# Kernel optimization log

Hardware: AMD Instinct MI355X
Metric: run time of the kernel (lower is better)

The kernel has to match this reference:

```python
import jax, jax.numpy as jnp
import numpy as np

T_LEN, BATCH, HID = 1024, 8, 1024
TEMP = 0.1
EPS = 1e-12  # torch F.normalize eps


def setup_inputs() -> dict:
    key = jax.random.key(0)
    k1, k2, k3, k4 = jax.random.split(key, 4)
    h1 = jax.random.normal(k1, (T_LEN, BATCH, HID), jnp.float32)
    h2 = jax.random.normal(k2, (T_LEN, BATCH, HID), jnp.float32)
    # learned params of nn.Sequential(Linear, ReLU, Linear, ReLU)
    W1 = jax.random.normal(k3, (HID, HID), jnp.float32) * 0.02
    b1 = jnp.zeros((HID,), jnp.float32)
    W2 = jax.random.normal(k4, (HID, HID), jnp.float32) * 0.02
    b2 = jnp.zeros((HID,), jnp.float32)
    return {"h1": h1, "h2": h2, "W1": W1, "b1": b1, "W2": W2, "b2": b2}


def _mlp(x, W1, b1, W2, b2):
    x = jax.nn.relu(x @ W1 + b1)
    return jax.nn.relu(x @ W2 + b2)


def _info_nce(emb_i, emb_j, temperature=TEMP):
    # emb_i, emb_j: [n, h] with n = 2*(t-1)
    n = emb_i.shape[0]
    z_i = emb_i / jnp.maximum(jnp.linalg.norm(emb_i, axis=1, keepdims=True), EPS)
    z_j = emb_j / jnp.maximum(jnp.linalg.norm(emb_j, axis=1, keepdims=True), EPS)
    reps = jnp.concatenate([z_i, z_j], axis=0)          # [2n, h]
    sim = reps @ reps.T                                  # cosine sim (rows are unit)
    logits = sim / temperature
    exp_l = jnp.exp(logits)
    # denominator excludes self-similarity (scatter of 0 at position i)
    denom = exp_l.sum(axis=1) - jnp.diagonal(exp_l)      # [2n]
    log_denom = jnp.log(denom)
    idx = jnp.arange(n)
    l_ab = -logits[idx, idx + n] + log_denom[:n]         # l(k, k+N)
    l_ba = -logits[idx + n, idx] + log_denom[n:]         # l(k+N, k)
    return (l_ab.sum() + l_ba.sum()) / (2.0 * n)


def reference(h1, h2, W1, b1, W2, b2):
    h1 = jnp.transpose(h1, (1, 0, 2))  # [b, t, h]
    h2 = jnp.transpose(h2, (1, 0, 2))
    h1 = _mlp(h1, W1, b1, W2, b2)
    h2 = _mlp(h2, W1, b1, W2, b2)
    h_t_1 = jnp.concatenate([h1[:, 1:, :], h2[:, 1:, :]], axis=1)    # [b, 2(t-1), h]
    h_t_2 = jnp.concatenate([h1[:, :-1, :], h2[:, :-1, :]], axis=1)
    # original loop overwrites cl_loss each iteration -> only last batch row counts
    cl_loss = _info_nce(h_t_1[-1], h_t_2[-1])
    return (h1, h2, cl_loss)
```

## Files before the change

### kernel.cpp

```cpp
#include <hip/hip_runtime.h>
#include <cstdint>
#include <cstddef>

using u16 = unsigned short;
using u8  = unsigned char;
typedef short short8 __attribute__((ext_vector_type(8)));
typedef __bf16 bf16x8 __attribute__((ext_vector_type(8)));
typedef float f32x4 __attribute__((ext_vector_type(4)));
typedef u16 u16x4 __attribute__((ext_vector_type(4)));
typedef int i32x4 __attribute__((ext_vector_type(4)));
typedef int i32x8 __attribute__((ext_vector_type(8)));

__device__ __forceinline__ u16 f2bf(float f) {
  union { float f; uint32_t u; } v; v.f = f;
  uint32_t r = v.u + 0x7FFF + ((v.u >> 16) & 1);
  return (u16)(r >> 16);
}
__device__ __forceinline__ float bf2f(u16 b) {
  union { uint32_t u; float f; } v; v.u = ((uint32_t)b) << 16;
  return v.f;
}
__device__ __forceinline__ u8 f2fp8(float f) {
  return (u8)(__builtin_amdgcn_cvt_pk_fp8_f32(f, f, 0, 0) & 0xFF);
}

__device__ __forceinline__ void gload16(const void* g, void* l) {
  __builtin_amdgcn_global_load_lds(
      (const __attribute__((address_space(1))) void*)g,
      (__attribute__((address_space(3))) void*)l, 16, 0, 0);
}

#define MFMAQ8(M0, N0, AF, BF)                                             \
  {                                                                        \
    _Pragma("unroll") for (int m_ = 0; m_ < 4; ++m_) {                     \
      _Pragma("unroll") for (int n_ = 0; n_ < 2; ++n_) {                   \
        acc[(M0) + m_][(N0) + n_] =                                        \
            __builtin_amdgcn_mfma_scale_f32_16x16x128_f8f6f4(              \
                AF[m_], BF[n_], acc[(M0) + m_][(N0) + n_],                 \
                0, 0, 0, 127, 0, 127);                                     \
      }                                                                    \
    }                                                                      \
  }

template <int EPI>
__global__ __launch_bounds__(512, 2) void gemm_fp8(
    const u8* __restrict__ A, const u8* __restrict__ Bt,
    const float* __restrict__ bias,
    u8* __restrict__ C8, float* __restrict__ Cf)
{
  constexpr int Kb = 1024, N = 1024, NT = 8;
  __shared__ alignas(16) u8 lds[131072];

  const int t = (int)threadIdx.x;
  const int lane = t & 63, wid = t >> 6;
  const int wr = wid >> 2, wc = wid & 3;
  const int li = lane & 15, hk = lane >> 4;

  const int orig = (int)blockIdx.x;
  const int cpx = (int)gridDim.x >> 3;
  const int swz = (orig & 7) * cpx + (orig >> 3);
  const int bm = swz >> 2, bn = swz & 3;
  const int arow0 = bm * 256, brow0 = bn * 256;

  const int Rl = lane >> 3;
  const int sc16 = ((lane & 7) ^ Rl) << 4;
  const int wid2 = wid * 2;

  const int c0b = (((hk << 1) + 0) ^ (li & 7)) << 4;
  const int c1b = (((hk << 1) + 1) ^ (li & 7)) << 4;

  f32x4 acc[8][4];
#pragma unroll
  for (int m = 0; m < 8; ++m)
#pragma unroll
    for (int n = 0; n < 4; ++n)
#pragma unroll
      for (int j = 0; j < 4; ++j) acc[m][n][j] = 0.0f;

  auto STAGE = [&](const u8* G, int growbase, int tau, int ldsoff) {
#pragma unroll
    for (int l = 0; l < 2; ++l) {
      const u8* g = G + (size_t)(growbase + (wid2 + l) * 8 + Rl) * Kb +
                    tau * 128 + sc16;
      gload16(g, lds + ldsoff + (wid2 + l) * 1024);
    }
  };
  auto RD = [&](const u8* base, int row) -> i32x8 {
    const u8* p = base + row * 128;
    i32x4 lo = *reinterpret_cast<const i32x4*>(p + c0b);
    i32x4 hi = *reinterpret_cast<const i32x4*>(p + c1b);
    i32x8 r;
    r[0] = lo[0]; r[1] = lo[1]; r[2] = lo[2]; r[3] = lo[3];
    r[4] = hi[0]; r[5] = hi[1]; r[6] = hi[2]; r[7] = hi[3];
    return r;
  };

  i32x8 aa[4], bb01[2], bb23[2];

  STAGE(Bt, brow0 + 0,   0, 65536 + 0);
  STAGE(Bt, brow0 + 128, 0, 65536 + 16384);
  STAGE(A,  arow0 + 0,   0, 0);
  STAGE(A,  arow0 + 128, 0, 16384);
  STAGE(Bt, brow0 + 0,   1, 65536 + 32768);
  STAGE(Bt, brow0 + 128, 1, 65536 + 32768 + 16384);
  STAGE(A,  arow0 + 0,   1, 32768);
  STAGE(A,  arow0 + 128, 1, 32768 + 16384);
  asm volatile("s_waitcnt vmcnt(8)" ::: "memory");
  __builtin_amdgcn_s_barrier();

  {
    const u8* Ab0 = lds + wr * 16384;
    const u8* Bb0 = lds + 65536 + wc * 8192;
#pragma unroll
    for (int m = 0; m < 4; ++m) aa[m] = RD(Ab0, m * 16 + li);
#pragma unroll
    for (int n = 0; n < 2; ++n) bb01[n] = RD(Bb0, n * 16 + li);
  }

  for (int tau = 0; tau < NT; ++tau) {
    const int cur = tau & 1, nxt = cur ^ 1;
    const u8* Ab  = lds + cur * 32768 + wr * 16384;
    const u8* Bb  = lds + 65536 + cur * 32768 + wc * 8192;
    const u8* Abn = lds + nxt * 32768 + wr * 16384;
    const u8* Bbn = lds + 65536 + nxt * 32768 + wc * 8192;

#pragma unroll
    for (int n = 0; n < 2; ++n) bb23[n] = RD(Bb, 32 + n * 16 + li);
    asm volatile("s_waitcnt lgkmcnt(4)" ::: "memory");
    __builtin_amdgcn_sched_barrier(0);
    __builtin_amdgcn_s_setprio(1);
    MFMAQ8(0, 0, aa, bb01);
    __builtin_amdgcn_s_setprio(0);

    asm volatile("s_waitcnt lgkmcnt(0)" ::: "memory");
    __builtin_amdgcn_sched_barrier(0);
    __builtin_amdgcn_s_setprio(1);
    MFMAQ8(0, 2, aa, bb23);
    __builtin_amdgcn_s_setprio(0);
    __builtin_amdgcn_sched_barrier(0);
#pragma unroll
    for (int m = 0; m < 4; ++m) aa[m] = RD(Ab, (m + 4) * 16 + li);
    __builtin_amdgcn_s_barrier();

    if (tau + 2 < NT) {
      STAGE(Bt, brow0 + 0,   tau + 2, 65536 + cur * 32768);
      STAGE(Bt, brow0 + 128, tau + 2, 65536 + cur * 32768 + 16384);
    }
    asm volatile("s_waitcnt lgkmcnt(0)" ::: "memory");
    __builtin_amdgcn_sched_barrier(0);
    __builtin_amdgcn_s_setprio(1);
    MFMAQ8(4, 2, aa, bb23);
    __builtin_amdgcn_s_setprio(0);
    __builtin_amdgcn_s_barrier();

    if (tau + 2 < NT) {
      STAGE(A, arow0 + 0,   tau + 2, cur * 32768);
      STAGE(A, arow0 + 128, tau + 2, cur * 32768 + 16384);
      asm volatile("s_waitcnt vmcnt(8)" ::: "memory");
    } else if (tau + 1 < NT) {
      asm volatile("s_waitcnt vmcnt(0)" ::: "memory");
    }
    __builtin_amdgcn_s_barrier();
    __builtin_amdgcn_s_setprio(1);
    MFMAQ8(4, 0, aa, bb01);
    __builtin_amdgcn_s_setprio(0);
    __builtin_amdgcn_sched_barrier(0);
    if (tau + 1 < NT) {
#pragma unroll
      for (int m = 0; m < 4; ++m) aa[m] = RD(Abn, m * 16 + li);
#pragma unroll
      for (int n = 0; n < 2; ++n) bb01[n] = RD(Bbn, n * 16 + li);
    }
  }

#pragma unroll
  for (int m = 0; m < 8; ++m) {
#pragma unroll
    for (int n = 0; n < 4; ++n) {
      const int gcol = brow0 + wc * 64 + n * 16 + li;
      const float bv = bias[gcol];
#pragma unroll
      for (int j = 0; j < 4; ++j) {
        const int grow = arow0 + wr * 128 + m * 16 + hk * 4 + j;
        float v = fmaxf(acc[m][n][j] * 0.001953125f + bv, 0.0f);
        if (EPI == 0) {
          C8[(size_t)grow * N + gcol] = f2fp8(v * 8.0f);
        } else {
          int tensor = grow >> 13, rr = grow & 8191;
          int tt = rr >> 3, b_ = rr & 7;
          Cf[(size_t)tensor * 8388608 + (size_t)b_ * 1048576 +
             (size_t)tt * 1024 + gcol] = v;
        }
      }
    }
  }
}

__global__ __launch_bounds__(256) void sim_kernel(const u16* __restrict__ Z,
                                                  float* __restrict__ S,
                                                  float* __restrict__ dots)
{
  __shared__ alignas(16) u16 As[128 * 128];
  __shared__ alignas(16) u16 Bs[128 * 128];
  const int t = (int)threadIdx.x;
  const int lane = t & 63, wv = t >> 6;
  const int wr = wv >> 1, wc = wv & 1;
  const int li = lane & 15, hk = lane >> 4;
  const int sr = t >> 4;
  const int scc = t & 15;
  const int bm = (int)blockIdx.x >> 4, bn = (int)blockIdx.x & 15;
  const int arow0 = bm * 128, brow0 = bn * 128;

  f32x4 acc[4][4];
#pragma unroll
  for (int m = 0; m < 4; ++m)
#pragma unroll
    for (int n = 0; n < 4; ++n)
#pragma unroll
      for (int j = 0; j < 4; ++j) acc[m][n][j] = 0.0f;

  for (int kt = 0; kt < 1024; kt += 128) {
#pragma unroll
    for (int l = 0; l < 8; ++l) {
      int row = l * 16 + sr;
      int coff = (scc ^ (row & 7)) << 3;
      const u16* ga = Z + (size_t)(arow0 + row) * 1024 + kt + coff;
      const u16* gb = Z + (size_t)(brow0 + row) * 1024 + kt + coff;
      gload16(ga, As + l * 2048 + wv * 512);
      gload16(gb, Bs + l * 2048 + wv * 512);
    }
    __syncthreads();
#pragma unroll
    for (int kk = 0; kk < 4; ++kk) {
      short8 av[4], bv[4];
#pragma unroll
      for (int m = 0; m < 4; ++m) {
        int ra = wr * 64 + m * 16 + li;
        int ca = ((kk << 2) + hk) ^ (ra & 7);
        av[m] = *reinterpret_cast<const short8*>(As + ra * 128 + ca * 8);
      }
#pragma unroll
      for (int n = 0; n < 4; ++n) {
        int rb = wc * 64 + n * 16 + li;
        int cb = ((kk << 2) + hk) ^ (rb & 7);
        bv[n] = *reinterpret_cast<const short8*>(Bs + rb * 128 + cb * 8);
      }
#pragma unroll
      for (int m = 0; m < 4; ++m)
#pragma unroll
        for (int n = 0; n < 4; ++n)
          acc[m][n] = __builtin_amdgcn_mfma_f32_16x16x32_bf16(
              __builtin_bit_cast(bf16x8, av[m]),
              __builtin_bit_cast(bf16x8, bv[n]),
              acc[m][n], 0, 0, 0);
    }
    __syncthreads();
  }

  float dsum = 0.0f;
#pragma unroll
  for (int m = 0; m < 4; ++m) {
#pragma unroll
    for (int j = 0; j < 4; ++j) {
      int grow = arow0 + wr * 64 + m * 16 + hk * 4 + j;
      float s = 0.0f;
#pragma unroll
      for (int n = 0; n < 4; ++n) {
        int gcol = brow0 + wc * 64 + n * 16 + li;
        float g = acc[m][n][j];
        float logit = (grow == gcol) ? 10.0f : g * 10.0f;
        float w = (gcol == 0 || gcol == 1023 || gcol == 1024 || gcol == 2047)
                      ? 1.0f : 2.0f;
        s += w * expf(logit);
        if (gcol == grow + 1 && (grow & 1023) != 1023) dsum += g;
      }
      s += __shfl_xor(s, 1); s += __shfl_xor(s, 2);
      s += __shfl_xor(s, 4); s += __shfl_xor(s, 8);
      if (li == 0) atomicAdd(&S[grow], s);
    }
  }
#pragma unroll
  for (int d = 1; d < 64; d <<= 1) dsum += __shfl_xor(dsum, d);
  if (lane == 0) atomicAdd(dots, dsum);
}

__global__ void prep_kernel(const float* __restrict__ h1,
                            const float* __restrict__ h2,
                            const float* __restrict__ W1,
                            const float* __restrict__ W2,
                            u8* __restrict__ X8,
                            u8* __restrict__ W1t,
                            u8* __restrict__ W2t,
                            float* __restrict__ S)
{
  __shared__ float tile[32][33];
  int bid = (int)blockIdx.x;
  if (bid < 16384) {
    size_t i4 = ((size_t)bid * 256 + threadIdx.x) * 4;
    const float* src = (i4 < 8388608) ? (h1 + i4) : (h2 + (i4 - 8388608));
    float4 v = *reinterpret_cast<const float4*>(src);
    int lo = __builtin_amdgcn_cvt_pk_fp8_f32(v.x * 8.0f, v.y * 8.0f, 0, 0);
    int all4 = __builtin_amdgcn_cvt_pk_fp8_f32(v.z * 8.0f, v.w * 8.0f, lo, 1);
    *reinterpret_cast<uint32_t*>(X8 + i4) = (uint32_t)all4;
    return;
  }
  bid -= 16384;
  const float* W;
  u8* Wt;
  if (bid < 1024) {
    W = W1; Wt = W1t;
  } else if (bid < 2048) {
    W = W2; Wt = W2t; bid -= 1024;
  } else {
    for (int i = (int)threadIdx.x; i < 2064; i += 256) S[i] = 0.0f;
    return;
  }
  const int bx = bid & 31, by = bid >> 5;
  const int tx = (int)threadIdx.x & 31, ty = (int)threadIdx.x >> 5;
#pragma unroll
  for (int i = 0; i < 4; ++i)
    tile[ty + i * 8][tx] = W[(size_t)(by * 32 + ty + i * 8) * 1024 + bx * 32 + tx];
  __syncthreads();
#pragma unroll
  for (int i = 0; i < 4; ++i)
    Wt[(size_t)(bx * 32 + ty + i * 8) * 1024 + by * 32 + tx] =
        f2fp8(tile[tx][ty + i * 8] * 64.0f);
}

__global__ void row_normalize(const float* __restrict__ out, u16* __restrict__ Z)
{
  const int row = (int)blockIdx.x;
  const int t = (int)threadIdx.x;
  const float* src = out + ((row < 1024)
      ? ((size_t)7 * 1048576 + (size_t)row * 1024)
      : ((size_t)8388608 + (size_t)7 * 1048576 + (size_t)(row - 1024) * 1024));
  float4 v = reinterpret_cast<const float4*>(src)[t];
  float ss = v.x * v.x + v.y * v.y + v.z * v.z + v.w * v.w;
#pragma unroll
  for (int d = 1; d < 64; d <<= 1) ss += __shfl_xor(ss, d);
  __shared__ float red[4];
  if ((t & 63) == 0) red[t >> 6] = ss;
  __syncthreads();
  float tot = red[0] + red[1] + red[2] + red[3];
  float inv = 1.0f / fmaxf(sqrtf(tot), 1e-12f);
  u16x4 o;
  o[0] = f2bf(v.x * inv); o[1] = f2bf(v.y * inv);
  o[2] = f2bf(v.z * inv); o[3] = f2bf(v.w * inv);
  reinterpret_cast<u16x4*>(Z + (size_t)row * 1024)[t] = o;
}

__global__ void finalize_kernel(const float* __restrict__ S,
                                const float* __restrict__ dots,
                                float* __restrict__ out_loss)
{
  const int t = (int)threadIdx.x;
  float acc = 0.0f;
  for (int i = t; i < 2048; i += 256) {
    int tl = i & 1023;
    float w = (tl == 0 || tl == 1023) ? 1.0f : 2.0f;
    acc += w * logf(S[i] - 22026.465794806718f);
  }
  __shared__ float red[256];
  red[t] = acc;
  __syncthreads();
  for (int s2 = 128; s2 > 0; s2 >>= 1) {
    if (t < s2) red[t] += red[t + s2];
    __syncthreads();
  }
  if (t == 0) out_loss[0] = (red[0] - 20.0f * dots[0]) / 4092.0f;
}

extern "C" void kernel_launch(void* const* d_in, const int* in_sizes, int n_in,
                              void* d_out, int out_size, void* d_ws, size_t ws_size,
                              hipStream_t stream)
{
  const float* h1 = (const float*)d_in[0];
  const float* h2 = (const float*)d_in[1];
  const float* W1 = (const float*)d_in[2];
  const float* b1 = (const float*)d_in[3];
  const float* W2 = (const float*)d_in[4];
  const float* b2 = (const float*)d_in[5];
  float* out = (float*)d_out;

  char* ws = (char*)d_ws;
  u8*    X8   = (u8*)ws;
  u8*    Y18  = (u8*)(ws + 16777216);
  u8*    W1t  = (u8*)(ws + 33554432);
  u8*    W2t  = (u8*)(ws + 34603008);
  u16*   Zb   = (u16*)(ws + 35651584);
  float* S    = (float*)(ws + 39845888);
  float* dots = S + 2048;

  prep_kernel<<<18433, 256, 0, stream>>>(h1, h2, W1, W2, X8, W1t, W2t, S);

  gemm_fp8<0><<<256, 512, 0, stream>>>(X8, W1t, b1, Y18, nullptr);
  gemm_fp8<1><<<256, 512, 0, stream>>>(Y18, W2t, b2, nullptr, out);

  row_normalize<<<2048, 256, 0, stream>>>(out, Zb);
  sim_kernel<<<256, 256, 0, stream>>>(Zb, S, dots);
  finalize_kernel<<<1, 256, 0, stream>>>(S, dots, out + 16777216);
}
```

Measured before the change: 104.3 us.

## Run the InfoNCE similarity GEMM in FP8 using the shared pipelined GEMM core

Row-normalized embeddings are now quantized to FP8 with a 16x scale instead of bf16, and the similarity matrix is computed by a new sim_fp8 kernel. This kernel reuses the pipelined FP8 MFMA core, factored out of gemm_fp8, with 256x256 tiles over 64 blocks of 512 threads. The goal is to halve the bytes the similarity kernel loads and to use the higher-throughput FP8 MFMA with the better-tuned pipeline. The risk is lower precision in the cosine similarities that feed the exp/log loss, and only 64 blocks on a GPU with many more compute units.

Result: slower. 193.6 us (+85.6%).

```diff
diff --git a/kernel.cpp b/kernel.cpp
--- a/kernel.cpp
+++ b/kernel.cpp
@@ -15,10 +15,6 @@
   union { float f; uint32_t u; } v; v.f = f;
   uint32_t r = v.u + 0x7FFF + ((v.u >> 16) & 1);
   return (u16)(r >> 16);
-}
-__device__ __forceinline__ float bf2f(u16 b) {
-  union { uint32_t u; float f; } v; v.u = ((uint32_t)b) << 16;
-  return v.f;
 }
 __device__ __forceinline__ u8 f2fp8(float f) {
   return (u8)(__builtin_amdgcn_cvt_pk_fp8_f32(f, f, 0, 0) & 0xFF);
@@ -42,40 +38,18 @@
     }                                                                      \
   }
 
-template <int EPI>
-__global__ __launch_bounds__(512, 2) void gemm_fp8(
+__device__ __forceinline__ void fp8_core(
     const u8* __restrict__ A, const u8* __restrict__ Bt,
-    const float* __restrict__ bias,
-    u8* __restrict__ C8, float* __restrict__ Cf)
-{
-  constexpr int Kb = 1024, N = 1024, NT = 8;
-  __shared__ alignas(16) u8 lds[131072];
-
-  const int t = (int)threadIdx.x;
-  const int lane = t & 63, wid = t >> 6;
-  const int wr = wid >> 2, wc = wid & 3;
-  const int li = lane & 15, hk = lane >> 4;
-
-  const int orig = (int)blockIdx.x;
-  const int cpx = (int)gridDim.x >> 3;
-  const int swz = (orig & 7) * cpx + (orig >> 3);
-  const int bm = swz >> 2, bn = swz & 3;
-  const int arow0 = bm * 256, brow0 = bn * 256;
-
+    int arow0, int brow0, u8* lds, f32x4 (&acc)[8][4],
+    int lane, int wid, int wr, int wc, int li)
+{
+  constexpr int Kb = 1024, NT = 8;
   const int Rl = lane >> 3;
   const int sc16 = ((lane & 7) ^ Rl) << 4;
   const int wid2 = wid * 2;
-
+  const int hk = lane >> 4;
   const int c0b = (((hk << 1) + 0) ^ (li & 7)) << 4;
   const int c1b = (((hk << 1) + 1) ^ (li & 7)) << 4;
-
-  f32x4 acc[8][4];
-#pragma unroll
-  for (int m = 0; m < 8; ++m)
-#pragma unroll
-    for (int n = 0; n < 4; ++n)
-#pragma unroll
-      for (int j = 0; j < 4; ++j) acc[m][n][j] = 0.0f;
 
   auto STAGE = [&](const u8* G, int growbase, int tau, int ldsoff) {
 #pragma unroll
@@ -172,6 +146,36 @@
       for (int n = 0; n < 2; ++n) bb01[n] = RD(Bbn, n * 16 + li);
     }
   }
+}
+
+template <int EPI>
+__global__ __launch_bounds__(512, 2) void gemm_fp8(
+    const u8* __restrict__ A, const u8* __restrict__ Bt,
+    const float* __restrict__ bias,
+    u8* __restrict__ C8, float* __restrict__ Cf)
+{
+  constexpr int N = 1024;
+  __shared__ alignas(16) u8 lds[131072];
+  const int t = (int)threadIdx.x;
+  const int lane = t & 63, wid = t >> 6;
+  const int wr = wid >> 2, wc = wid & 3;
+  const int li = lane & 15, hk = lane >> 4;
+
+  const int orig = (int)blockIdx.x;
+  const int cpx = (int)gridDim.x >> 3;
+  const int swz = (orig & 7) * cpx + (orig >> 3);
+  const int bm = swz >> 2, bn = swz & 3;
+  const int arow0 = bm * 256, brow0 = bn * 256;
+
+  f32x4 acc[8][4];
+#pragma unroll
+  for (int m = 0; m < 8; ++m)
+#pragma unroll
+    for (int n = 0; n < 4; ++n)
+#pragma unroll
+      for (int j = 0; j < 4; ++j) acc[m][n][j] = 0.0f;
+
+  fp8_core(A, Bt, arow0, brow0, lds, acc, lane, wid, wr, wc, li);
 
 #pragma unroll
   for (int m = 0; m < 8; ++m) {
@@ -196,78 +200,41 @@
   }
 }
 
-__global__ __launch_bounds__(256) void sim_kernel(const u16* __restrict__ Z,
-                                                  float* __restrict__ S,
-                                                  float* __restrict__ dots)
-{
-  __shared__ alignas(16) u16 As[128 * 128];
-  __shared__ alignas(16) u16 Bs[128 * 128];
+__global__ __launch_bounds__(512, 2) void sim_fp8(
+    const u8* __restrict__ Z8, float* __restrict__ S, float* __restrict__ dots)
+{
+  __shared__ alignas(16) u8 lds[131072];
   const int t = (int)threadIdx.x;
-  const int lane = t & 63, wv = t >> 6;
-  const int wr = wv >> 1, wc = wv & 1;
+  const int lane = t & 63, wid = t >> 6;
+  const int wr = wid >> 2, wc = wid & 3;
   const int li = lane & 15, hk = lane >> 4;
-  const int sr = t >> 4;
-  const int scc = t & 15;
-  const int bm = (int)blockIdx.x >> 4, bn = (int)blockIdx.x & 15;
-  const int arow0 = bm * 128, brow0 = bn * 128;
-
-  f32x4 acc[4][4];
-#pragma unroll
-  for (int m = 0; m < 4; ++m)
+
+  const int orig = (int)blockIdx.x;
+  const int swz = (orig & 7) * 8 + (orig >> 3);
+  const int bm = swz >> 3, bn = swz & 7;
+  const int arow0 = bm * 256, brow0 = bn * 256;
+
+  f32x4 acc[8][4];
+#pragma unroll
+  for (int m = 0; m < 8; ++m)
 #pragma unroll
     for (int n = 0; n < 4; ++n)
 #pragma unroll
       for (int j = 0; j < 4; ++j) acc[m][n][j] = 0.0f;
 
-  for (int kt = 0; kt < 1024; kt += 128) {
-#pragma unroll
-    for (int l = 0; l < 8; ++l) {
-      int row = l * 16 + sr;
-      int coff = (scc ^ (row & 7)) << 3;
-      const u16* ga = Z + (size_t)(arow0 + row) * 1024 + kt + coff;
-      const u16* gb = Z + (size_t)(brow0 + row) * 1024 + kt + coff;
-      gload16(ga, As + l * 2048 + wv * 512);
-      gload16(gb, Bs + l * 2048 + wv * 512);
-    }
-    __syncthreads();
-#pragma unroll
-    for (int kk = 0; kk < 4; ++kk) {
-      short8 av[4], bv[4];
-#pragma unroll
-      for (int m = 0; m < 4; ++m) {
-        int ra = wr * 64 + m * 16 + li;
-        int ca = ((kk << 2) + hk) ^ (ra & 7);
-        av[m] = *reinterpret_cast<const short8*>(As + ra * 128 + ca * 8);
-      }
+  fp8_core(Z8, Z8, arow0, brow0, lds, acc, lane, wid, wr, wc, li);
+
+  float dsum = 0.0f;
+#pragma unroll
+  for (int m = 0; m < 8; ++m) {
+#pragma unroll
+    for (int j = 0; j < 4; ++j) {
+      const int grow = arow0 + wr * 128 + m * 16 + hk * 4 + j;
+      float s = 0.0f;
 #pragma unroll
       for (int n = 0; n < 4; ++n) {
-        int rb = wc * 64 + n * 16 + li;
-        int cb = ((kk << 2) + hk) ^ (rb & 7);
-        bv[n] = *reinterpret_cast<const short8*>(Bs + rb * 128 + cb * 8);
-      }
-#pragma unroll
-      for (int m = 0; m < 4; ++m)
-#pragma unroll
-        for (int n = 0; n < 4; ++n)
-          acc[m][n] = __builtin_amdgcn_mfma_f32_16x16x32_bf16(
-              __builtin_bit_cast(bf16x8, av[m]),
-              __builtin_bit_cast(bf16x8, bv[n]),
-              acc[m][n], 0, 0, 0);
-    }
-    __syncthreads();
-  }
-
-  float dsum = 0.0f;
-#pragma unroll
-  for (int m = 0; m < 4; ++m) {
-#pragma unroll
-    for (int j = 0; j < 4; ++j) {
-      int grow = arow0 + wr * 64 + m * 16 + hk * 4 + j;
-      float s = 0.0f;
-#pragma unroll
-      for (int n = 0; n < 4; ++n) {
-        int gcol = brow0 + wc * 64 + n * 16 + li;
-        float g = acc[m][n][j];
+        const int gcol = brow0 + wc * 64 + n * 16 + li;
+        const float g = acc[m][n][j] * 0.00390625f;
         float logit = (grow == gcol) ? 10.0f : g * 10.0f;
         float w = (gcol == 0 || gcol == 1023 || gcol == 1024 || gcol == 2047)
                       ? 1.0f : 2.0f;
@@ -327,7 +294,7 @@
         f2fp8(tile[tx][ty + i * 8] * 64.0f);
 }
 
-__global__ void row_normalize(const float* __restrict__ out, u16* __restrict__ Z)
+__global__ void row_normalize(const float* __restrict__ out, u8* __restrict__ Z8)
 {
   const int row = (int)blockIdx.x;
   const int t = (int)threadIdx.x;
@@ -342,11 +309,10 @@
   if ((t & 63) == 0) red[t >> 6] = ss;
   __syncthreads();
   float tot = red[0] + red[1] + red[2] + red[3];
-  float inv = 1.0f / fmaxf(sqrtf(tot), 1e-12f);
-  u16x4 o;
-  o[0] = f2bf(v.x * inv); o[1] = f2bf(v.y * inv);
-  o[2] = f2bf(v.z * inv); o[3] = f2bf(v.w * inv);
-  reinterpret_cast<u16x4*>(Z + (size_t)row * 1024)[t] = o;
+  float inv = 16.0f / fmaxf(sqrtf(tot), 1e-12f);
+  int lo = __builtin_amdgcn_cvt_pk_fp8_f32(v.x * inv, v.y * inv, 0, 0);
+  int all4 = __builtin_amdgcn_cvt_pk_fp8_f32(v.z * inv, v.w * inv, lo, 1);
+  reinterpret_cast<uint32_t*>(Z8 + (size_t)row * 1024)[t] = (uint32_t)all4;
 }
 
 __global__ void finalize_kernel(const float* __restrict__ S,
@@ -387,8 +353,8 @@
   u8*    Y18  = (u8*)(ws + 16777216);
   u8*    W1t  = (u8*)(ws + 33554432);
   u8*    W2t  = (u8*)(ws + 34603008);
-  u16*   Zb   = (u16*)(ws + 35651584);
-  float* S    = (float*)(ws + 39845888);
+  u8*    Z8   = (u8*)(ws + 35651584);
+  float* S    = (float*)(ws + 37748736);
   float* dots = S + 2048;
 
   prep_kernel<<<18433, 256, 0, stream>>>(h1, h2, W1, W2, X8, W1t, W2t, S);
@@ -396,7 +362,7 @@
   gemm_fp8<0><<<256, 512, 0, stream>>>(X8, W1t, b1, Y18, nullptr);
   gemm_fp8<1><<<256, 512, 0, stream>>>(Y18, W2t, b2, nullptr, out);
 
-  row_normalize<<<2048, 256, 0, stream>>>(out, Zb);
-  sim_kernel<<<256, 256, 0, stream>>>(Zb, S, dots);
+  row_normalize<<<2048, 256, 0, stream>>>(out, Z8);
+  sim_fp8<<<64, 512, 0, stream>>>(Z8, S, dots);
   finalize_kernel<<<1, 256, 0, stream>>>(S, dots, out + 16777216);
 }
```
